# Optimization experiments

Measured on AMD Instinct MI355X. Metric: run time of the kernel, lower is better.

## Reference

```python
import jax, jax.numpy as jnp
import numpy as np

B, T, C, H = 4, 2048, 768, 12
D = C // H

def setup_inputs() -> dict:
    key = jax.random.key(0)
    ks = jax.random.split(key, 8)
    s = 1.0 / np.sqrt(C)
    return {
        "x":  jax.random.normal(ks[0], (B, T, C), dtype=jnp.float32),
        "Wq": jax.random.normal(ks[1], (C, C), dtype=jnp.float32) * s,
        "bq": jax.random.normal(ks[2], (C,), dtype=jnp.float32) * 0.02,
        "Wk": jax.random.normal(ks[3], (C, C), dtype=jnp.float32) * s,
        "bk": jax.random.normal(ks[4], (C,), dtype=jnp.float32) * 0.02,
        "Wv": jax.random.normal(ks[5], (C, C), dtype=jnp.float32) * s,
        "bv": jax.random.normal(ks[6], (C,), dtype=jnp.float32) * 0.02,
        "Wp": jax.random.normal(ks[7], (C, C), dtype=jnp.float32) * s,
    }

def reference(x, Wq, bq, Wk, bk, Wv, bv, Wp):
    # Linear projections (torch Linear: y = x @ W.T + b)
    q = x @ Wq.T + bq
    k = x @ Wk.T + bk
    v = x @ Wv.T + bv
    # [B,T,C] -> [B,H,T,D]
    q = q.reshape(B, T, H, D).transpose(0, 2, 1, 3)
    k = k.reshape(B, T, H, D).transpose(0, 2, 1, 3)
    v = v.reshape(B, T, H, D).transpose(0, 2, 1, 3)
    scale = 1.0 / np.sqrt(D).astype(np.float32)
    scores = jnp.einsum('bhqd,bhkd->bhqk', q, k) * scale  # [B,H,T,T]
    attn = jax.nn.softmax(scores, axis=-1)  # no mask in original module
    out = jnp.einsum('bhqk,bhkd->bhqd', attn, v)
    out = out.transpose(0, 2, 1, 3).reshape(B, T, C)
    return out @ Wp.T  # proj has bias=False
```

## Files before the change

### kernel.cpp

```cpp
#include <hip/hip_runtime.h>
#include <hip/hip_bf16.h>
#include <cmath>

constexpr int B  = 4;
constexpr int T  = 2048;
constexpr int C  = 768;
constexpr int H  = 12;
constexpr int Dh = 64;
constexpr int M  = B * T;
constexpr int NQKV = 3 * C;
constexpr int WS2  = C * C;

typedef short bf16x8 __attribute__((ext_vector_type(8)));
typedef short bf16x4 __attribute__((ext_vector_type(4)));
typedef float f32x4  __attribute__((ext_vector_type(4)));

__device__ inline short f2bf(float f) {
    unsigned u = __float_as_uint(f);
    u += 0x7fffu + ((u >> 16) & 1u);
    return (short)(u >> 16);
}

__device__ inline unsigned pk_bf16(float a, float b) {
    __hip_bfloat162 h = __float22bfloat162_rn(float2{a, b});
    return *(unsigned*)&h;
}

typedef const __attribute__((address_space(1))) unsigned GU;
typedef __attribute__((address_space(3))) unsigned LU;
__device__ inline void async_copy16(const void* g, void* l) {
    __builtin_amdgcn_global_load_lds((GU*)g, (LU*)l, 16, 0, 0);
}

constexpr size_t XE = (size_t)M * C;
constexpr size_t CV_TOTAL = XE + 4 * (size_t)WS2;

__global__ __launch_bounds__(256)
void convert_all(const float* __restrict__ x,  const float* __restrict__ Wq,
                 const float* __restrict__ Wk, const float* __restrict__ Wv,
                 const float* __restrict__ Wp,
                 short* __restrict__ xb, short* __restrict__ Wqkv,
                 short* __restrict__ Wpb) {
    size_t i = ((size_t)blockIdx.x * 256 + threadIdx.x) * 4;
    const float* src; short* dst; size_t off;
    if (i < XE)                    { src = x;  dst = xb;            off = i; }
    else if (i < XE + WS2)         { src = Wq; dst = Wqkv;          off = i - XE; }
    else if (i < XE + 2 * (size_t)WS2) { src = Wk; dst = Wqkv + WS2;     off = i - XE - WS2; }
    else if (i < XE + 3 * (size_t)WS2) { src = Wv; dst = Wqkv + 2 * WS2; off = i - XE - 2 * (size_t)WS2; }
    else                           { src = Wp; dst = Wpb;           off = i - XE - 3 * (size_t)WS2; }
    float4 v = *(const float4*)(src + off);
    bf16x4 o; o[0] = f2bf(v.x); o[1] = f2bf(v.y); o[2] = f2bf(v.z); o[3] = f2bf(v.w);
    *(bf16x4*)(dst + off) = o;
}

constexpr int BM = 128, BK = 32;

template<int BN_, int WMW, int WNW, int OUT_BF16>
__global__ __launch_bounds__(256)
void gemm_bt(const short* __restrict__ A, const short* __restrict__ W,
             const float* __restrict__ bias0, const float* __restrict__ bias1,
             const float* __restrict__ bias2,
             void* __restrict__ Yv, int Ndim, int Kdim) {
    constexpr int MT = BM / WMW / 16;
    constexpr int NT = BN_ / WNW / 16;
    constexpr int NCHUNK = (BM + BN_) / 16;
    __shared__ short As[BM * BK];
    __shared__ short Bs[BN_ * BK];

    const int tid  = threadIdx.x;
    const int wave = tid >> 6;
    const int lane = tid & 63;
    const int li   = lane & 15;
    const int quad = lane >> 4;
    const int wm   = wave % WMW;
    const int wn   = wave / WMW;
    const int m0   = blockIdx.y * BM;
    const int n0   = blockIdx.x * BN_;

    f32x4 acc[MT][NT];
    #pragma unroll
    for (int i = 0; i < MT; ++i)
        #pragma unroll
        for (int j = 0; j < NT; ++j)
            acc[i][j] = (f32x4){0.f, 0.f, 0.f, 0.f};

    const int lrow = lane >> 2;
    const int lkof = (lane & 3) * 8;

    for (int k0 = 0; k0 < Kdim; k0 += BK) {
        __syncthreads();
        #pragma unroll
        for (int ii = 0; ii < NCHUNK / 4; ++ii) {
            int c = ii * 4 + wave;
            if (c < BM / 16)
                async_copy16(A + (size_t)(m0 + c * 16 + lrow) * Kdim + k0 + lkof,
                             &As[c * 512]);
            else
                async_copy16(W + (size_t)(n0 + (c - BM / 16) * 16 + lrow) * Kdim + k0 + lkof,
                             &Bs[(c - BM / 16) * 512]);
        }
        __syncthreads();

        bf16x8 af[MT], bfr[NT];
        #pragma unroll
        for (int t = 0; t < MT; ++t)
            af[t] = *(const bf16x8*)&As[(wm * MT * 16 + t * 16 + li) * BK + quad * 8];
        #pragma unroll
        for (int t = 0; t < NT; ++t)
            bfr[t] = *(const bf16x8*)&Bs[(wn * NT * 16 + t * 16 + li) * BK + quad * 8];
        #pragma unroll
        for (int i = 0; i < MT; ++i)
            #pragma unroll
            for (int j = 0; j < NT; ++j)
                acc[i][j] = __builtin_amdgcn_mfma_f32_16x16x32_bf16(
                    af[i], bfr[j], acc[i][j], 0, 0, 0);
    }

    float bb[NT];
    #pragma unroll
    for (int nt = 0; nt < NT; ++nt) bb[nt] = 0.f;
    if (bias0) {
        int s = n0 / C;
        const float* bp = (s == 0) ? bias0 : ((s == 1) ? bias1 : bias2);
        int nb = n0 % C;
        #pragma unroll
        for (int nt = 0; nt < NT; ++nt)
            bb[nt] = bp[nb + wn * NT * 16 + nt * 16 + li];
    }

    #pragma unroll
    for (int mt = 0; mt < MT; ++mt)
        #pragma unroll
        for (int nt = 0; nt < NT; ++nt)
            #pragma unroll
            for (int r = 0; r < 4; ++r) {
                int row = m0 + wm * MT * 16 + mt * 16 + quad * 4 + r;
                int col = n0 + wn * NT * 16 + nt * 16 + li;
                float v = acc[mt][nt][r] + bb[nt];
                if constexpr (OUT_BF16)
                    ((short*)Yv)[(size_t)row * Ndim + col] = f2bf(v);
                else
                    ((float*)Yv)[(size_t)row * Ndim + col] = v;
            }
}

constexpr int QT   = 128;
constexpr int KTT  = 64;
constexpr int LSTR = 72;
constexpr int PSTR = 72;
constexpr int QS   = NQKV;
constexpr float SOFT_SCALE = 0.18033688011112042f;

__global__ __launch_bounds__(256)
void attn_fwd(const short* __restrict__ QKV, short* __restrict__ O) {
    __shared__ short Vt[2][Dh * LSTR];
    __shared__ short Ps[4 * 32 * PSTR];

    const int tid  = threadIdx.x;
    const int wave = tid >> 6;
    const int lane = tid & 63;
    const int li   = lane & 15;
    const int quad = lane >> 4;
    const int b    = blockIdx.z;
    const int h    = blockIdx.y;
    const int qw   = blockIdx.x * QT + wave * 32;

    const short* Qg = QKV + (size_t)(b * T) * QS + h * Dh;
    const short* Kg = QKV + (size_t)(b * T) * QS + C + h * Dh;
    const short* Vg = QKV + (size_t)(b * T) * QS + 2 * C + h * Dh;

    bf16x8 qf[2][2];
    #pragma unroll
    for (int qb = 0; qb < 2; ++qb)
        #pragma unroll
        for (int dh = 0; dh < 2; ++dh)
            qf[qb][dh] = *(const bf16x8*)(Qg + (size_t)(qw + qb * 16 + li) * QS
                                             + dh * 32 + quad * 8);

    bf16x8 ones;
    #pragma unroll
    for (int i = 0; i < 8; ++i) ones[i] = (short)0x3F80;

    f32x4 oacc[2][4];
    #pragma unroll
    for (int qb = 0; qb < 2; ++qb)
        #pragma unroll
        for (int db = 0; db < 4; ++db)
            oacc[qb][db] = (f32x4){0.f, 0.f, 0.f, 0.f};
    f32x4 lacc[2] = {(f32x4){0.f, 0.f, 0.f, 0.f}, (f32x4){0.f, 0.f, 0.f, 0.f}};

    const int vd2 = (tid & 31) * 2;
    const int vg  = tid >> 5;

    unsigned vpre[8];
    #pragma unroll
    for (int t2 = 0; t2 < 8; ++t2)
        vpre[t2] = *(const unsigned*)(Vg + (size_t)(vg * 8 + t2) * QS + vd2);

    for (int kt = 0; kt < T; kt += KTT) {
        const int p = (kt >> 6) & 1;

        {
            bf16x8 vlo, vhi;
            #pragma unroll
            for (int t2 = 0; t2 < 8; ++t2) {
                vlo[t2] = (short)(vpre[t2] & 0xffffu);
                vhi[t2] = (short)(vpre[t2] >> 16);
            }
            *(bf16x8*)&Vt[p][vd2 * LSTR + vg * 8]       = vlo;
            *(bf16x8*)&Vt[p][(vd2 + 1) * LSTR + vg * 8] = vhi;
        }
        __syncthreads();

        if (kt + KTT < T) {
            #pragma unroll
            for (int t2 = 0; t2 < 8; ++t2)
                vpre[t2] = *(const unsigned*)(Vg + (size_t)(kt + KTT + vg * 8 + t2) * QS + vd2);
        }

        f32x4 st[2][4];
        #pragma unroll
        for (int kb = 0; kb < 4; ++kb) {
            const short* kr = Kg + (size_t)(kt + kb * 16 + li) * QS + quad * 8;
            bf16x8 kf0 = *(const bf16x8*)kr;
            bf16x8 kf1 = *(const bf16x8*)(kr + 32);
            #pragma unroll
            for (int qb = 0; qb < 2; ++qb) {
                f32x4 a = (f32x4){0.f, 0.f, 0.f, 0.f};
                a = __builtin_amdgcn_mfma_f32_16x16x32_bf16(kf0, qf[qb][0], a, 0, 0, 0);
                a = __builtin_amdgcn_mfma_f32_16x16x32_bf16(kf1, qf[qb][1], a, 0, 0, 0);
                st[qb][kb] = a;
            }
        }

        #pragma unroll
        for (int qb = 0; qb < 2; ++qb)
            #pragma unroll
            for (int kb = 0; kb < 4; ++kb) {
                float p0 = exp2f(st[qb][kb][0] * SOFT_SCALE);
                float p1 = exp2f(st[qb][kb][1] * SOFT_SCALE);
                float p2 = exp2f(st[qb][kb][2] * SOFT_SCALE);
                float p3 = exp2f(st[qb][kb][3] * SOFT_SCALE);
                uint2 w; w.x = pk_bf16(p0, p1); w.y = pk_bf16(p2, p3);
                *(uint2*)&Ps[(wave * 32 + qb * 16 + li) * PSTR + kb * 16 + quad * 4] = w;
            }
        __asm__ volatile("s_waitcnt lgkmcnt(0)" ::: "memory");

        #pragma unroll
        for (int kq = 0; kq < 2; ++kq) {
            bf16x8 pf[2];
            #pragma unroll
            for (int qb = 0; qb < 2; ++qb) {
                pf[qb] = *(const bf16x8*)&Ps[(wave * 32 + qb * 16 + li) * PSTR
                                             + kq * 32 + quad * 8];
                lacc[qb] = __builtin_amdgcn_mfma_f32_16x16x32_bf16(
                    pf[qb], ones, lacc[qb], 0, 0, 0);
            }
            #pragma unroll
            for (int db = 0; db < 4; ++db) {
                bf16x8 vf = *(const bf16x8*)&Vt[p][(db * 16 + li) * LSTR + kq * 32 + quad * 8];
                #pragma unroll
                for (int qb = 0; qb < 2; ++qb)
                    oacc[qb][db] = __builtin_amdgcn_mfma_f32_16x16x32_bf16(
                        pf[qb], vf, oacc[qb][db], 0, 0, 0);
            }
        }
    }

    #pragma unroll
    for (int qb = 0; qb < 2; ++qb)
        #pragma unroll
        for (int r = 0; r < 4; ++r) {
            float inv = 1.0f / lacc[qb][r];
            short* op = O + (size_t)(b * T + qw + qb * 16 + quad * 4 + r) * C
                          + h * Dh + li;
            #pragma unroll
            for (int db = 0; db < 4; ++db)
                op[db * 16] = f2bf(oacc[qb][db][r] * inv);
        }
}

extern "C" void kernel_launch(void* const* d_in, const int* in_sizes, int n_in,
                              void* d_out, int out_size, void* d_ws, size_t ws_size,
                              hipStream_t stream) {
    (void)in_sizes; (void)n_in; (void)out_size; (void)ws_size;

    const float* x  = (const float*)d_in[0];
    const float* Wq = (const float*)d_in[1];
    const float* bq = (const float*)d_in[2];
    const float* Wk = (const float*)d_in[3];
    const float* bk = (const float*)d_in[4];
    const float* Wv = (const float*)d_in[5];
    const float* bv = (const float*)d_in[6];
    const float* Wp = (const float*)d_in[7];
    float* out = (float*)d_out;

    short* xb    = (short*)d_ws;
    short* Wqkv  = xb + (size_t)M * C;
    short* Wpb   = Wqkv + 3 * (size_t)WS2;
    short* QKVb  = Wpb + (size_t)WS2;
    short* AOb   = QKVb + (size_t)M * NQKV;

    convert_all<<<dim3(CV_TOTAL / 1024), 256, 0, stream>>>(
        x, Wq, Wk, Wv, Wp, xb, Wqkv, Wpb);

    gemm_bt<128, 2, 2, 1><<<dim3(NQKV / 128, M / BM), 256, 0, stream>>>(
        xb, Wqkv, bq, bk, bv, QKVb, NQKV, C);

    attn_fwd<<<dim3(T / QT, H, B), 256, 0, stream>>>(QKVb, AOb);

    gemm_bt<64, 4, 1, 0><<<dim3(C / 64, M / BM), 256, 0, stream>>>(
        AOb, Wpb, nullptr, nullptr, nullptr, out, C, C);
}
```

Measured before the change: 283.8 us.

## Stage K tiles in shared memory and single-buffer V in attention

Each block now loads the K tile cooperatively into LDS with register prefetch and reads MFMA K fragments from LDS, instead of every wave loading K directly from global memory. V goes from a double buffer to a single buffer guarded by a barrier at the top of each iteration. The V transpose is packed with byte-permute instructions, and exp2f is replaced by the hardware exp2 builtin. The intent is to cut redundant global K traffic and ALU work, at the cost of an extra barrier per tile and more LDS use.

```diff
diff --git a/kernel.cpp b/kernel.cpp
--- a/kernel.cpp
+++ b/kernel.cpp
@@ -43,11 +43,11 @@
                  short* __restrict__ Wpb) {
     size_t i = ((size_t)blockIdx.x * 256 + threadIdx.x) * 4;
     const float* src; short* dst; size_t off;
-    if (i < XE)                    { src = x;  dst = xb;            off = i; }
-    else if (i < XE + WS2)         { src = Wq; dst = Wqkv;          off = i - XE; }
-    else if (i < XE + 2 * (size_t)WS2) { src = Wk; dst = Wqkv + WS2;     off = i - XE - WS2; }
+    if (i < XE)                        { src = x;  dst = xb;            off = i; }
+    else if (i < XE + WS2)             { src = Wq; dst = Wqkv;          off = i - XE; }
+    else if (i < XE + 2 * (size_t)WS2) { src = Wk; dst = Wqkv + WS2;    off = i - XE - WS2; }
     else if (i < XE + 3 * (size_t)WS2) { src = Wv; dst = Wqkv + 2 * WS2; off = i - XE - 2 * (size_t)WS2; }
-    else                           { src = Wp; dst = Wpb;           off = i - XE - 3 * (size_t)WS2; }
+    else                               { src = Wp; dst = Wpb;           off = i - XE - 3 * (size_t)WS2; }
     float4 v = *(const float4*)(src + off);
     bf16x4 o; o[0] = f2bf(v.x); o[1] = f2bf(v.y); o[2] = f2bf(v.z); o[3] = f2bf(v.w);
     *(bf16x4*)(dst + off) = o;
@@ -153,7 +153,8 @@
 
 __global__ __launch_bounds__(256)
 void attn_fwd(const short* __restrict__ QKV, short* __restrict__ O) {
-    __shared__ short Vt[2][Dh * LSTR];
+    __shared__ short Ks[KTT * LSTR];
+    __shared__ short Vt[Dh * LSTR];
     __shared__ short Ps[4 * 32 * PSTR];
 
     const int tid  = threadIdx.x;
@@ -189,41 +190,50 @@
             oacc[qb][db] = (f32x4){0.f, 0.f, 0.f, 0.f};
     f32x4 lacc[2] = {(f32x4){0.f, 0.f, 0.f, 0.f}, (f32x4){0.f, 0.f, 0.f, 0.f}};
 
-    const int vd2 = (tid & 31) * 2;
-    const int vg  = tid >> 5;
-
+    const int ktok = tid >> 3;
+    const int kch  = tid & 7;
+    const int vd2  = (tid & 31) * 2;
+    const int vg   = tid >> 5;
+
+    int4 kpre[2];
     unsigned vpre[8];
+    kpre[0] = *(const int4*)(Kg + (size_t)(ktok)      * QS + kch * 8);
+    kpre[1] = *(const int4*)(Kg + (size_t)(ktok + 32) * QS + kch * 8);
     #pragma unroll
     for (int t2 = 0; t2 < 8; ++t2)
         vpre[t2] = *(const unsigned*)(Vg + (size_t)(vg * 8 + t2) * QS + vd2);
 
     for (int kt = 0; kt < T; kt += KTT) {
-        const int p = (kt >> 6) & 1;
-
+        __syncthreads();
+
+        *(int4*)&Ks[ktok * LSTR + kch * 8]        = kpre[0];
+        *(int4*)&Ks[(ktok + 32) * LSTR + kch * 8] = kpre[1];
         {
-            bf16x8 vlo, vhi;
-            #pragma unroll
-            for (int t2 = 0; t2 < 8; ++t2) {
-                vlo[t2] = (short)(vpre[t2] & 0xffffu);
-                vhi[t2] = (short)(vpre[t2] >> 16);
-            }
-            *(bf16x8*)&Vt[p][vd2 * LSTR + vg * 8]       = vlo;
-            *(bf16x8*)&Vt[p][(vd2 + 1) * LSTR + vg * 8] = vhi;
+            unsigned lo[4], hi[4];
+            #pragma unroll
+            for (int j = 0; j < 4; ++j) {
+                lo[j] = __builtin_amdgcn_perm(vpre[2 * j + 1], vpre[2 * j], 0x05040100u);
+                hi[j] = __builtin_amdgcn_perm(vpre[2 * j + 1], vpre[2 * j], 0x07060302u);
+            }
+            *(int4*)&Vt[vd2 * LSTR + vg * 8]       = make_int4(lo[0], lo[1], lo[2], lo[3]);
+            *(int4*)&Vt[(vd2 + 1) * LSTR + vg * 8] = make_int4(hi[0], hi[1], hi[2], hi[3]);
         }
         __syncthreads();
 
         if (kt + KTT < T) {
+            const size_t nb = kt + KTT;
+            kpre[0] = *(const int4*)(Kg + (nb + ktok)      * QS + kch * 8);
+            kpre[1] = *(const int4*)(Kg + (nb + ktok + 32) * QS + kch * 8);
             #pragma unroll
             for (int t2 = 0; t2 < 8; ++t2)
-                vpre[t2] = *(const unsigned*)(Vg + (size_t)(kt + KTT + vg * 8 + t2) * QS + vd2);
+                vpre[t2] = *(const unsigned*)(Vg + (nb + vg * 8 + t2) * QS + vd2);
         }
 
         f32x4 st[2][4];
         #pragma unroll
         for (int kb = 0; kb < 4; ++kb) {
-            const short* kr = Kg + (size_t)(kt + kb * 16 + li) * QS + quad * 8;
-            bf16x8 kf0 = *(const bf16x8*)kr;
-            bf16x8 kf1 = *(const bf16x8*)(kr + 32);
+            bf16x8 kf0 = *(const bf16x8*)&Ks[(kb * 16 + li) * LSTR + quad * 8];
+            bf16x8 kf1 = *(const bf16x8*)&Ks[(kb * 16 + li) * LSTR + 32 + quad * 8];
             #pragma unroll
             for (int qb = 0; qb < 2; ++qb) {
                 f32x4 a = (f32x4){0.f, 0.f, 0.f, 0.f};
@@ -237,10 +247,10 @@
         for (int qb = 0; qb < 2; ++qb)
             #pragma unroll
             for (int kb = 0; kb < 4; ++kb) {
-                float p0 = exp2f(st[qb][kb][0] * SOFT_SCALE);
-                float p1 = exp2f(st[qb][kb][1] * SOFT_SCALE);
-                float p2 = exp2f(st[qb][kb][2] * SOFT_SCALE);
-                float p3 = exp2f(st[qb][kb][3] * SOFT_SCALE);
+                float p0 = __builtin_amdgcn_exp2f(st[qb][kb][0] * SOFT_SCALE);
+                float p1 = __builtin_amdgcn_exp2f(st[qb][kb][1] * SOFT_SCALE);
+                float p2 = __builtin_amdgcn_exp2f(st[qb][kb][2] * SOFT_SCALE);
+                float p3 = __builtin_amdgcn_exp2f(st[qb][kb][3] * SOFT_SCALE);
                 uint2 w; w.x = pk_bf16(p0, p1); w.y = pk_bf16(p2, p3);
                 *(uint2*)&Ps[(wave * 32 + qb * 16 + li) * PSTR + kb * 16 + quad * 4] = w;
             }
@@ -258,7 +268,7 @@
             }
             #pragma unroll
             for (int db = 0; db < 4; ++db) {
-                bf16x8 vf = *(const bf16x8*)&Vt[p][(db * 16 + li) * LSTR + kq * 32 + quad * 8];
+                bf16x8 vf = *(const bf16x8*)&Vt[(db * 16 + li) * LSTR + kq * 32 + quad * 8];
                 #pragma unroll
                 for (int qb = 0; qb < 2; ++qb)
                     oacc[qb][db] = __builtin_amdgcn_mfma_f32_16x16x32_bf16(
```

Result: faster. 247.5 us (-12.8%).
